# Optimization experiments

Measured on AMD Instinct MI355X. Metric: run time of the kernel, lower is better.

The kernel has to match this reference:

```python
import jax, jax.numpy as jnp
import numpy as np

LEVEL_SHAPES = ((128, 128), (64, 64), (32, 32), (16, 16))  # (H_l, W_l) per level
B, LQ, C, H, L, P, DFF = 4, 1024, 256, 8, 4, 4, 1024
DH = C // H
LSRC = sum(h * w for h, w in LEVEL_SHAPES)
NORMALIZER = np.array([[w, h] for h, w in LEVEL_SHAPES], dtype=np.float32)  # (L,2) as (W,H)


def layer_norm(x, g, b, eps=1e-5):
    m = jnp.mean(x, -1, keepdims=True)
    v = jnp.var(x, -1, keepdims=True)
    return (x - m) * jax.lax.rsqrt(v + eps) * g + b


def mha(tgt, query_pos, w_in, b_in, w_out, b_out):
    # nn.MultiheadAttention with q=k=tgt+pos, v=tgt (eval mode, no dropout)
    qk = tgt + query_pos
    q = (qk @ w_in[:C].T + b_in[:C]).reshape(B, LQ, H, DH)
    k = (qk @ w_in[C:2 * C].T + b_in[C:2 * C]).reshape(B, LQ, H, DH)
    v = (tgt @ w_in[2 * C:].T + b_in[2 * C:]).reshape(B, LQ, H, DH)
    att = jax.nn.softmax(jnp.einsum('bqhd,bkhd->bhqk', q, k) / np.float32(np.sqrt(DH)), axis=-1)
    o = jnp.einsum('bhqk,bkhd->bqhd', att, v).reshape(B, LQ, C)
    return o @ w_out.T + b_out


def ms_deform_attn(query, ref, src, off_w, off_b, aw_w, aw_b, val_w, val_b, out_w, out_b):
    value = (src @ val_w.T + val_b).reshape(B, LSRC, H, DH)
    offsets = (query @ off_w.T + off_b).reshape(B, LQ, H, L, P, 2)
    aw = jax.nn.softmax((query @ aw_w.T + aw_b).reshape(B, LQ, H, L * P), axis=-1)
    aw = aw.reshape(B, LQ, H, L, P)
    # sampling locations in [0,1], offsets normalized per level by (W_l, H_l)
    loc = ref[:, :, None, :, None, :] + offsets / NORMALIZER[None, None, None, :, None, :]
    out = jnp.zeros((B, LQ, H, DH), query.dtype)
    start = 0
    for l, (h, w) in enumerate(LEVEL_SHAPES):
        v = value[:, start:start + h * w].reshape(B, h, w, H, DH)
        v = v.transpose(0, 3, 1, 2, 4).reshape(B, H, h * w, DH)  # [B,H,hw,DH]
        start += h * w
        # grid_sample semantics: align_corners=False, zero padding
        x = loc[:, :, :, l, :, 0] * w - 0.5  # [B,LQ,H,P]
        y = loc[:, :, :, l, :, 1] * h - 0.5
        x0 = jnp.floor(x); y0 = jnp.floor(y)
        x0i = x0.astype(jnp.int32); y0i = y0.astype(jnp.int32)
        wx1 = x - x0; wx0 = 1.0 - wx1
        wy1 = y - y0; wy0 = 1.0 - wy1

        def gather(ix, iy):
            valid = ((ix >= 0) & (ix < w) & (iy >= 0) & (iy < h)).astype(v.dtype)
            idx = jnp.clip(iy, 0, h - 1) * w + jnp.clip(ix, 0, w - 1)
            idx = idx.transpose(0, 2, 1, 3).reshape(B, H, LQ * P)
            g = jnp.take_along_axis(v, idx[..., None], axis=2).reshape(B, H, LQ, P, DH)
            return g * valid.transpose(0, 2, 1, 3)[..., None]

        def wmul(ww):
            return ww.transpose(0, 2, 1, 3)[..., None]  # [B,H,LQ,P,1]

        s = (gather(x0i, y0i) * wmul(wx0 * wy0)
             + gather(x0i + 1, y0i) * wmul(wx1 * wy0)
             + gather(x0i, y0i + 1) * wmul(wx0 * wy1)
             + gather(x0i + 1, y0i + 1) * wmul(wx1 * wy1))
        out = out + jnp.einsum('bhqpd,bqhp->bqhd', s, aw[:, :, :, l])
    return out.reshape(B, LQ, C) @ out_w.T + out_b


def setup_inputs():
    key = jax.random.key(0)
    ks = jax.random.split(key, 16)

    def n(i, shape, s=0.02):
        return jax.random.normal(ks[i], shape, jnp.float32) * s

    z = lambda *s: jnp.zeros(s, jnp.float32)
    o = lambda *s: jnp.ones(s, jnp.float32)
    return {
        'tgt': n(0, (B, LQ, C), 1.0),
        'query_pos': n(1, (B, LQ, C), 1.0),
        'reference_points': jax.random.uniform(ks[2], (B, LQ, L, 2), jnp.float32),
        'src': n(3, (B, LSRC, C), 1.0),
        'in_w': n(4, (3 * C, C)), 'in_b': z(3 * C),
        'sa_w': n(5, (C, C)), 'sa_b': z(C),
        'off_w': n(6, (H * L * P * 2, C)), 'off_b': n(7, (H * L * P * 2,), 2.0),
        'aw_w': n(8, (H * L * P, C)), 'aw_b': z(H * L * P),
        'val_w': n(9, (C, C)), 'val_b': z(C),
        'co_w': n(10, (C, C)), 'co_b': z(C),
        'ln1_g': o(C), 'ln1_b': z(C),
        'ln2_g': o(C), 'ln2_b': z(C),
        'ln3_g': o(C), 'ln3_b': z(C),
        'f1_w': n(11, (DFF, C)), 'f1_b': z(DFF),
        'f2_w': n(12, (C, DFF)), 'f2_b': z(C),
    }


def reference(tgt, query_pos, reference_points, src, in_w, in_b, sa_w, sa_b,
              off_w, off_b, aw_w, aw_b, val_w, val_b, co_w, co_b,
              ln1_g, ln1_b, ln2_g, ln2_b, ln3_g, ln3_b,
              f1_w, f1_b, f2_w, f2_b):
    # self-attention + residual + norm2
    tgt2 = mha(tgt, query_pos, in_w, in_b, sa_w, sa_b)
    tgt = layer_norm(tgt + tgt2, ln2_g, ln2_b)
    # multi-scale deformable cross-attention + residual + norm1 (DETR path)
    tgt2 = ms_deform_attn(tgt + query_pos, reference_points, src,
                          off_w, off_b, aw_w, aw_b, val_w, val_b, co_w, co_b)
    tgt = layer_norm(tgt + tgt2, ln1_g, ln1_b)
    # FFN + residual + norm3
    tgt2 = jax.nn.relu(tgt @ f1_w.T + f1_b) @ f2_w.T + f2_b
    tgt = layer_norm(tgt + tgt2, ln3_g, ln3_b)
    return tgt
```

## Files before the change

kernel.cpp:

```cpp
#include <hip/hip_runtime.h>
#include <hip/hip_bf16.h>
#include <math.h>

#define Bv   4
#define LQv  1024
#define Cv   256
#define Hv   8
#define Lv   4
#define Pv   4
#define DFFv 1024
#define DHv  32
#define LSRCv 21760

typedef __attribute__((ext_vector_type(8))) short bhalf8;
typedef __attribute__((ext_vector_type(4))) float floatx4;

__device__ inline unsigned pk_bf16x2(float x, float y) {
    unsigned xb = __float_as_uint(x), yb = __float_as_uint(y);
    unsigned xr = (xb + 0x7FFFu + ((xb >> 16) & 1u)) >> 16;
    unsigned yr = (yb + 0x7FFFu + ((yb >> 16) & 1u)) >> 16;
    return xr | (yr << 16);
}
__device__ inline unsigned short bf16_1(float x) {
    unsigned xb = __float_as_uint(x);
    return (unsigned short)((xb + 0x7FFFu + ((xb >> 16) & 1u)) >> 16);
}
__device__ inline float ubf2f(unsigned short u) {
    return __uint_as_float(((unsigned)u) << 16);
}

__global__ __launch_bounds__(256) void cvt_weights(const float* __restrict__ in_w,
                                                   const float* __restrict__ sa_w,
                                                   const float* __restrict__ val_w,
                                                   const float* __restrict__ off_w,
                                                   const float* __restrict__ aw_w,
                                                   const float* __restrict__ co_w,
                                                   const float* __restrict__ f1_w,
                                                   const float* __restrict__ f2_w,
                                                   const float* __restrict__ off_b,
                                                   const float* __restrict__ aw_b,
                                                   unsigned short* __restrict__ wp,
                                                   float* __restrict__ cbias) {
    const size_t idx4 = (size_t)blockIdx.x * 256 + threadIdx.x;
    if (idx4 >= 253952) {
        const int t = (int)(idx4 - 253952);
        if (t < 256) cbias[t] = off_b[t];
        else if (t < 384) cbias[t] = aw_b[t - 256];
        return;
    }
    const size_t f = idx4 * 4;
    const float* src; size_t off; int K; size_t obase; int nadd = 0;
    if (f < 196608)      { src = in_w;  off = f;          K = 256;  obase = 0; }
    else if (f < 262144) { src = sa_w;  off = f - 196608; K = 256;  obase = 196608; }
    else if (f < 327680) { src = val_w; off = f - 262144; K = 256;  obase = 262144; }
    else if (f < 393216) { src = off_w; off = f - 327680; K = 256;  obase = 327680; }
    else if (f < 425984) { src = aw_w;  off = f - 393216; K = 256;  obase = 327680; nadd = 256; }
    else if (f < 491520) { src = co_w;  off = f - 425984; K = 256;  obase = 425984; }
    else if (f < 753664) { src = f1_w;  off = f - 491520; K = 256;  obase = 491520; }
    else                 { src = f2_w;  off = f - 753664; K = 1024; obase = 753664; }
    float4 v = *(const float4*)(src + off);
    const int n = (int)(off / (size_t)K) + nadd, k = (int)(off % (size_t)K);
    const size_t di = obase + ((size_t)((n >> 4) * (K >> 5) + (k >> 5))) * 512
                    + (size_t)(((k >> 3) & 3) * 128 + (n & 15) * 8 + (k & 7));
    *(uint2*)(wp + di) = (uint2){pk_bf16x2(v.x, v.y), pk_bf16x2(v.z, v.w)};
}

struct GJob {
    const float* A; const float* A2;
    const unsigned short* Wp; const float* bias;
    float* Cf; unsigned short* Ch;
    int M, N, K, relu;
};

__device__ __forceinline__ void gemm_body(unsigned short* AsBase,
                                          const float* __restrict__ A,
                                          const float* __restrict__ A2,
                                          const unsigned short* __restrict__ Wp,
                                          const float* __restrict__ bias,
                                          float* __restrict__ Cf,
                                          unsigned short* __restrict__ Ch,
                                          int N, int K, int relu, unsigned bid) {
    const unsigned nc = (unsigned)N >> 6;
    const unsigned xcd = bid & 7, j = bid >> 3;
    const unsigned cpan = j % nc, r8 = j / nc;
    const int bm = (int)((xcd + (r8 << 3)) << 6);
    const int bn = (int)(cpan << 6);
    const int tid = threadIdx.x;
    const int wid = tid >> 6, lane = tid & 63;
    const int wr = wid >> 1, wc = wid & 1;
    const int col16 = lane & 15;
    const int quad = lane >> 4;

    const int srow0 = tid >> 4;
    const int scol = (tid & 15) * 4;
    const float* asrc = A + (size_t)(bm + srow0) * K + scol;
    const float* a2src = A2 ? A2 + (size_t)(bm + srow0) * K + scol : nullptr;

    const int K32 = K >> 5;
    const unsigned short* wbase = Wp + ((size_t)((bn >> 4) + wc * 2) * K32) * 512
                                + (size_t)lane * 8;

    floatx4 acc[2][2] = {};
    float4 rv[4][2];

    auto loadA = [&](int c) {
#pragma unroll
        for (int j2 = 0; j2 < 4; ++j2)
#pragma unroll
            for (int i = 0; i < 2; ++i)
                rv[j2][i] = *(const float4*)(asrc + (size_t)(16 * j2) * K + c * 128 + 64 * i);
        if (a2src) {
#pragma unroll
            for (int j2 = 0; j2 < 4; ++j2)
#pragma unroll
                for (int i = 0; i < 2; ++i) {
                    float4 t = *(const float4*)(a2src + (size_t)(16 * j2) * K + c * 128 + 64 * i);
                    rv[j2][i].x += t.x; rv[j2][i].y += t.y;
                    rv[j2][i].z += t.z; rv[j2][i].w += t.w;
                }
        }
    };
    auto writeA = [&](int buf) {
        unsigned short* dst = AsBase + buf * (64 * 136);
#pragma unroll
        for (int j2 = 0; j2 < 4; ++j2)
#pragma unroll
            for (int i = 0; i < 2; ++i) {
                uint2 p = {pk_bf16x2(rv[j2][i].x, rv[j2][i].y),
                           pk_bf16x2(rv[j2][i].z, rv[j2][i].w)};
                *(uint2*)&dst[(srow0 + 16 * j2) * 136 + scol + 64 * i] = p;
            }
    };

    const int NC = K >> 7;
    loadA(0);
    writeA(0);

    for (int c = 0; c < NC; ++c) {
        __syncthreads();
        if (c + 1 < NC) loadA(c + 1);

        const unsigned short* ab = AsBase + (c & 1) * (64 * 136);
#pragma unroll
        for (int s = 0; s < 4; ++s) {
            bhalf8 bfr[2];
#pragma unroll
            for (int nt = 0; nt < 2; ++nt)
                bfr[nt] = *(const bhalf8*)(wbase + ((size_t)(nt * K32 + c * 4 + s)) * 512);
            bhalf8 af[2];
#pragma unroll
            for (int mt = 0; mt < 2; ++mt)
                af[mt] = *(const bhalf8*)&ab[(wr * 32 + mt * 16 + col16) * 136 + s * 32 + quad * 8];
#pragma unroll
            for (int mt = 0; mt < 2; ++mt)
#pragma unroll
                for (int nt = 0; nt < 2; ++nt)
                    acc[mt][nt] = __builtin_amdgcn_mfma_f32_16x16x32_bf16(
                        af[mt], bfr[nt], acc[mt][nt], 0, 0, 0);
        }

        if (c + 1 < NC) writeA((c + 1) & 1);
    }

#pragma unroll
    for (int mt = 0; mt < 2; ++mt) {
#pragma unroll
        for (int nt = 0; nt < 2; ++nt) {
            const int col = bn + wc * 32 + nt * 16 + col16;
            const float bv = bias[col];
#pragma unroll
            for (int i = 0; i < 4; ++i) {
                const int row = bm + wr * 32 + mt * 16 + quad * 4 + i;
                float v = acc[mt][nt][i] + bv;
                if (relu) v = fmaxf(v, 0.f);
                if (Ch) Ch[(size_t)row * N + col] = bf16_1(v);
                else    Cf[(size_t)row * N + col] = v;
            }
        }
    }
}

__global__ __launch_bounds__(256, 4) void gemm_single(const float* __restrict__ A,
                                                      const float* __restrict__ A2,
                                                      const unsigned short* __restrict__ Wp,
                                                      const float* __restrict__ bias,
                                                      float* __restrict__ Cf,
                                                      unsigned short* __restrict__ Ch,
                                                      int N, int K, int relu) {
    __shared__ __attribute__((aligned(16))) unsigned short As[2 * 64 * 136];
    gemm_body(As, A, A2, Wp, bias, Cf, Ch, N, K, relu, blockIdx.x);
}

__global__ __launch_bounds__(256, 4) void gemm_triple(GJob j0, GJob j1, GJob j2,
                                                      unsigned c0, unsigned c01) {
    __shared__ __attribute__((aligned(16))) unsigned short As[2 * 64 * 136];
    const unsigned b = blockIdx.x;
    if (b < c0) {
        gemm_body(As, j0.A, j0.A2, j0.Wp, j0.bias, j0.Cf, j0.Ch, j0.N, j0.K, j0.relu, b);
    } else if (b < c01) {
        gemm_body(As, j1.A, j1.A2, j1.Wp, j1.bias, j1.Cf, j1.Ch, j1.N, j1.K, j1.relu, b - c0);
    } else {
        gemm_body(As, j2.A, j2.A2, j2.Wp, j2.bias, j2.Cf, j2.Ch, j2.N, j2.K, j2.relu, b - c01);
    }
}

#define ATT_SCALE 0.17677669529663687f
__global__ __launch_bounds__(256, 2) void attn_mfma(const float* __restrict__ Q,
                                                    const float* __restrict__ Kb,
                                                    const float* __restrict__ Vb,
                                                    float* __restrict__ O,
                                                    int qk_stride) {
    const int b = blockIdx.z, h = blockIdx.y, qt = blockIdx.x;
    const int tid = threadIdx.x;
    const int wid = tid >> 6, lane = tid & 63;
    const int col16 = lane & 15, quad = lane >> 4;

    __shared__ unsigned short smem_us[40960];
    unsigned short* Ks = smem_us + wid * 9600;
    unsigned short* Vt = Ks + 2560;
    unsigned short* Ps = Ks + 4864;
    float* corr_s = (float*)(Ks + 9472);
    unsigned short* Qs = smem_us + 38400;

    {
        const int row = tid >> 2, part = tid & 3;
        const float* qsrc = Q + ((size_t)(b * LQv + qt * 64 + row)) * qk_stride + h * DHv + part * 8;
        float4 qa = *(const float4*)qsrc;
        float4 qb2 = *(const float4*)(qsrc + 4);
        uint4 qp = {pk_bf16x2(qa.x * ATT_SCALE, qa.y * ATT_SCALE),
                    pk_bf16x2(qa.z * ATT_SCALE, qa.w * ATT_SCALE),
                    pk_bf16x2(qb2.x * ATT_SCALE, qb2.y * ATT_SCALE),
                    pk_bf16x2(qb2.z * ATT_SCALE, qb2.w * ATT_SCALE)};
        *(uint4*)&Qs[row * 40 + part * 8] = qp;
    }
    __syncthreads();
    bhalf8 qfr[4];
#pragma unroll
    for (int j = 0; j < 4; ++j)
        qfr[j] = *(const bhalf8*)&Qs[(j * 16 + col16) * 40 + quad * 8];

    float m_state[4] = {-1e30f, -1e30f, -1e30f, -1e30f};
    float l_state[4] = {0.f, 0.f, 0.f, 0.f};
    floatx4 acc_o[4][2] = {};
    const int dd = lane & 31, half = lane >> 5;

    const float* kbase = Kb + ((size_t)(b * LQv + wid * 256)) * qk_stride + h * DHv;
    const float* vbase = Vb + ((size_t)(b * LQv + wid * 256)) * Cv + h * DHv;

#pragma unroll 1
    for (int t = 0; t < 4; ++t) {
        {
            const float* ks = kbase + (size_t)(t * 64 + lane) * qk_stride;
            float4 f0 = *(const float4*)(ks + 0),  f1 = *(const float4*)(ks + 4);
            float4 f2 = *(const float4*)(ks + 8),  f3 = *(const float4*)(ks + 12);
            float4 f4 = *(const float4*)(ks + 16), f5 = *(const float4*)(ks + 20);
            float4 f6 = *(const float4*)(ks + 24), f7 = *(const float4*)(ks + 28);
            uint4 p0 = {pk_bf16x2(f0.x, f0.y), pk_bf16x2(f0.z, f0.w),
                        pk_bf16x2(f1.x, f1.y), pk_bf16x2(f1.z, f1.w)};
            uint4 p1 = {pk_bf16x2(f2.x, f2.y), pk_bf16x2(f2.z, f2.w),
                        pk_bf16x2(f3.x, f3.y), pk_bf16x2(f3.z, f3.w)};
            uint4 p2 = {pk_bf16x2(f4.x, f4.y), pk_bf16x2(f4.z, f4.w),
                        pk_bf16x2(f5.x, f5.y), pk_bf16x2(f5.z, f5.w)};
            uint4 p3 = {pk_bf16x2(f6.x, f6.y), pk_bf16x2(f6.z, f6.w),
                        pk_bf16x2(f7.x, f7.y), pk_bf16x2(f7.z, f7.w)};
            *(uint4*)&Ks[lane * 40 + 0]  = p0;
            *(uint4*)&Ks[lane * 40 + 8]  = p1;
            *(uint4*)&Ks[lane * 40 + 16] = p2;
            *(uint4*)&Ks[lane * 40 + 24] = p3;
        }
        {
            const float* vs = vbase + (size_t)(t * 64 + half * 32) * Cv + dd;
#pragma unroll
            for (int j4 = 0; j4 < 8; ++j4) {
                float g0 = vs[(j4 * 4 + 0) * Cv], g1 = vs[(j4 * 4 + 1) * Cv];
                float g2 = vs[(j4 * 4 + 2) * Cv], g3 = vs[(j4 * 4 + 3) * Cv];
                uint2 vp = {pk_bf16x2(g0, g1), pk_bf16x2(g2, g3)};
                *(uint2*)&Vt[dd * 72 + half * 32 + j4 * 4] = vp;
            }
        }

        floatx4 accs[4][4] = {};
        bhalf8 af[4];
#pragma unroll
        for (int kf = 0; kf < 4; ++kf)
            af[kf] = *(const bhalf8*)&Ks[(kf * 16 + col16) * 40 + quad * 8];
#pragma unroll
        for (int kf = 0; kf < 4; ++kf)
#pragma unroll
            for (int qf = 0; qf < 4; ++qf)
                accs[kf][qf] = __builtin_amdgcn_mfma_f32_16x16x32_bf16(
                    af[kf], qfr[qf], accs[kf][qf], 0, 0, 0);

#pragma unroll
        for (int qf = 0; qf < 4; ++qf) {
            float tmax = -1e30f;
#pragma unroll
            for (int kf = 0; kf < 4; ++kf) {
                tmax = fmaxf(tmax, fmaxf(fmaxf(accs[kf][qf][0], accs[kf][qf][1]),
                                         fmaxf(accs[kf][qf][2], accs[kf][qf][3])));
            }
            tmax = fmaxf(tmax, __shfl_xor(tmax, 16));
            tmax = fmaxf(tmax, __shfl_xor(tmax, 32));
            float mnew = fmaxf(m_state[qf], tmax);
            float cr = __expf(m_state[qf] - mnew);
            m_state[qf] = mnew;
            float psum = 0.f;
#pragma unroll
            for (int kf = 0; kf < 4; ++kf) {
                float p0 = __expf(accs[kf][qf][0] - mnew);
                float p1 = __expf(accs[kf][qf][1] - mnew);
                float p2 = __expf(accs[kf][qf][2] - mnew);
                float p3 = __expf(accs[kf][qf][3] - mnew);
                psum += (p0 + p1) + (p2 + p3);
                uint2 pp = {pk_bf16x2(p0, p1), pk_bf16x2(p2, p3)};
                *(uint2*)&Ps[(qf * 16 + col16) * 72 + kf * 16 + quad * 4] = pp;
            }
            psum += __shfl_xor(psum, 16);
            psum += __shfl_xor(psum, 32);
            l_state[qf] = l_state[qf] * cr + psum;
            if (quad == 0) corr_s[qf * 16 + col16] = cr;
        }

#pragma unroll
        for (int mf = 0; mf < 4; ++mf) {
            float4 cv = *(const float4*)&corr_s[mf * 16 + quad * 4];
#pragma unroll
            for (int nf = 0; nf < 2; ++nf) {
                acc_o[mf][nf][0] *= cv.x;
                acc_o[mf][nf][1] *= cv.y;
                acc_o[mf][nf][2] *= cv.z;
                acc_o[mf][nf][3] *= cv.w;
            }
        }
#pragma unroll
        for (int ks2 = 0; ks2 < 2; ++ks2) {
            bhalf8 pf[4], vf[2];
#pragma unroll
            for (int mf = 0; mf < 4; ++mf)
                pf[mf] = *(const bhalf8*)&Ps[(mf * 16 + col16) * 72 + ks2 * 32 + quad * 8];
#pragma unroll
            for (int nf = 0; nf < 2; ++nf)
                vf[nf] = *(const bhalf8*)&Vt[(nf * 16 + col16) * 72 + ks2 * 32 + quad * 8];
#pragma unroll
            for (int mf = 0; mf < 4; ++mf)
#pragma unroll
                for (int nf = 0; nf < 2; ++nf)
                    acc_o[mf][nf] = __builtin_amdgcn_mfma_f32_16x16x32_bf16(
                        pf[mf], vf[nf], acc_o[mf][nf], 0, 0, 0);
        }
    }

    __syncthreads();
    float* mbuf = (float*)smem_us;
    float* lbuf = mbuf + 256;
    float* obuf = lbuf + 256;
    if (quad == 0) {
#pragma unroll
        for (int qf = 0; qf < 4; ++qf) {
            mbuf[wid * 64 + qf * 16 + col16] = m_state[qf];
            lbuf[wid * 64 + qf * 16 + col16] = l_state[qf];
        }
    }
#pragma unroll
    for (int mf = 0; mf < 4; ++mf)
#pragma unroll
        for (int nf = 0; nf < 2; ++nf)
#pragma unroll
            for (int i = 0; i < 4; ++i)
                obuf[wid * 2048 + (mf * 16 + quad * 4 + i) * 32 + nf * 16 + col16] =
                    acc_o[mf][nf][i];
    __syncthreads();
    {
        const int q = tid >> 2, dg = (tid & 3) * 8;
        float m0 = mbuf[q], m1 = mbuf[64 + q], m2 = mbuf[128 + q], m3 = mbuf[192 + q];
        float gm = fmaxf(fmaxf(m0, m1), fmaxf(m2, m3));
        float e0 = __expf(m0 - gm), e1 = __expf(m1 - gm);
        float e2 = __expf(m2 - gm), e3 = __expf(m3 - gm);
        float lt = lbuf[q] * e0 + lbuf[64 + q] * e1 + lbuf[128 + q] * e2 + lbuf[192 + q] * e3;
        float inv = 1.f / lt;
        const float* o0 = obuf + q * 32 + dg;
        float* orow = O + ((size_t)(b * LQv + qt * 64 + q)) * Cv + h * DHv + dg;
        float ov[8];
#pragma unroll
        for (int d = 0; d < 8; ++d)
            ov[d] = (o0[d] * e0 + o0[2048 + d] * e1 + o0[4096 + d] * e2 + o0[6144 + d] * e3) * inv;
        *(float4*)(orow) = make_float4(ov[0], ov[1], ov[2], ov[3]);
        *(float4*)(orow + 4) = make_float4(ov[4], ov[5], ov[6], ov[7]);
    }
}

__global__ __launch_bounds__(256) void deform_sample(const unsigned short* __restrict__ value,
                                                     const float* __restrict__ oab,
                                                     const float* __restrict__ ref,
                                                     float* __restrict__ out) {
    const int bq = blockIdx.x;
    const int b = bq >> 10;
    const int tid = threadIdx.x;
    const int h = tid >> 5, d = tid & 31;

    const float* aw = oab + (size_t)bq * 384 + 256 + h * 16;
    float w[16];
    float mx = -1e30f;
#pragma unroll
    for (int j = 0; j < 16; ++j) { w[j] = aw[j]; mx = fmaxf(mx, w[j]); }
    float ssum = 0.f;
#pragma unroll
    for (int j = 0; j < 16; ++j) { w[j] = __expf(w[j] - mx); ssum += w[j]; }
    float invs = 1.f / ssum;

    const float* op = oab + (size_t)bq * 384 + h * 32;
    const float* rp = ref + (size_t)bq * (Lv * 2);

    const int starts[4] = {0, 16384, 20480, 21504};
    const int WHl[4] = {128, 64, 32, 16};

    float acc = 0.f;
#pragma unroll 1
    for (int l = 0; l < 4; ++l) {
        const int wl = WHl[l];
        const float rx = rp[l * 2 + 0], ry = rp[l * 2 + 1];
        const unsigned short* vb0 = value + ((size_t)b * LSRCv + starts[l]) * Cv + h * DHv + d;
#pragma unroll 1
        for (int p = 0; p < 4; ++p) {
            float ox = op[l * 8 + p * 2 + 0], oy = op[l * 8 + p * 2 + 1];
            float x = rx * (float)wl + ox - 0.5f;
            float y = ry * (float)wl + oy - 0.5f;
            float fx0 = floorf(x), fy0 = floorf(y);
            int x0 = (int)fx0, y0 = (int)fy0;
            float tx = x - fx0, ty = y - fy0;
            float w00 = (1.f - tx) * (1.f - ty);
            float w10 = tx * (1.f - ty);
            float w01 = (1.f - tx) * ty;
            float w11 = tx * ty;
            float s = 0.f;
            bool xin0 = (x0 >= 0) & (x0 < wl);
            bool xin1 = (x0 + 1 >= 0) & (x0 + 1 < wl);
            bool yin0 = (y0 >= 0) & (y0 < wl);
            bool yin1 = (y0 + 1 >= 0) & (y0 + 1 < wl);
            if (yin0) {
                if (xin0) s = fmaf(w00, ubf2f(vb0[(size_t)(y0 * wl + x0) * Cv]), s);
                if (xin1) s = fmaf(w10, ubf2f(vb0[(size_t)(y0 * wl + x0 + 1) * Cv]), s);
            }
            if (yin1) {
                if (xin0) s = fmaf(w01, ubf2f(vb0[(size_t)((y0 + 1) * wl + x0) * Cv]), s);
                if (xin1) s = fmaf(w11, ubf2f(vb0[(size_t)((y0 + 1) * wl + x0 + 1) * Cv]), s);
            }
            acc = fmaf(w[l * 4 + p] * invs, s, acc);
        }
    }
    out[(size_t)bq * Cv + h * DHv + d] = acc;
}

__global__ __launch_bounds__(256) void ln_residual(const float* __restrict__ x,
                                                   const float* __restrict__ r,
                                                   const float* __restrict__ g,
                                                   const float* __restrict__ bta,
                                                   float* __restrict__ out) {
    const int row = blockIdx.x;
    const int tid = threadIdx.x;
    float v = x[(size_t)row * Cv + tid] + r[(size_t)row * Cv + tid];
    float s = v, sq = v * v;
#pragma unroll
    for (int off = 32; off > 0; off >>= 1) {
        s  += __shfl_down(s, off, 64);
        sq += __shfl_down(sq, off, 64);
    }
    __shared__ float ss[4], sqq[4];
    int wid = tid >> 6;
    if ((tid & 63) == 0) { ss[wid] = s; sqq[wid] = sq; }
    __syncthreads();
    __shared__ float meansh, rstdsh;
    if (tid == 0) {
        float S = ss[0] + ss[1] + ss[2] + ss[3];
        float Q = sqq[0] + sqq[1] + sqq[2] + sqq[3];
        float mean = S * (1.f / Cv);
        float var = Q * (1.f / Cv) - mean * mean;
        meansh = mean;
        rstdsh = rsqrtf(var + 1e-5f);
    }
    __syncthreads();
    out[(size_t)row * Cv + tid] = (v - meansh) * rstdsh * g[tid] + bta[tid];
}

extern "C" void kernel_launch(void* const* d_in, const int* in_sizes, int n_in,
                              void* d_out, int out_size, void* d_ws, size_t ws_size,
                              hipStream_t stream) {
    const float* tgt       = (const float*)d_in[0];
    const float* query_pos = (const float*)d_in[1];
    const float* ref_pts   = (const float*)d_in[2];
    const float* src       = (const float*)d_in[3];
    const float* in_w      = (const float*)d_in[4];
    const float* in_b      = (const float*)d_in[5];
    const float* sa_w      = (const float*)d_in[6];
    const float* sa_b      = (const float*)d_in[7];
    const float* off_w     = (const float*)d_in[8];
    const float* off_b     = (const float*)d_in[9];
    const float* aw_w      = (const float*)d_in[10];
    const float* aw_b      = (const float*)d_in[11];
    const float* val_w     = (const float*)d_in[12];
    const float* val_b     = (const float*)d_in[13];
    const float* co_w      = (const float*)d_in[14];
    const float* co_b      = (const float*)d_in[15];
    const float* ln1_g     = (const float*)d_in[16];
    const float* ln1_b     = (const float*)d_in[17];
    const float* ln2_g     = (const float*)d_in[18];
    const float* ln2_b     = (const float*)d_in[19];
    const float* ln3_g     = (const float*)d_in[20];
    const float* ln3_b     = (const float*)d_in[21];
    const float* f1_w      = (const float*)d_in[22];
    const float* f1_b      = (const float*)d_in[23];
    const float* f2_w      = (const float*)d_in[24];
    const float* f2_b      = (const float*)d_in[25];

    const int M0  = Bv * LQv * Cv;
    const int VSZ = Bv * LSRCv * Cv;
    float* ws = (float*)d_ws;

    float* big    = ws;
    float* qkbuf  = big;
    float* vb     = big + (size_t)2 * M0;
    float* ob     = big + (size_t)3 * M0;
    unsigned short* value16 = (unsigned short*)(big + (size_t)4 * M0);
    unsigned short* wb = (unsigned short*)(big + (size_t)20000000);
    float* cbias  = big + (size_t)20510000;
    float* tgt_a  = ws + (size_t)VSZ;
    float* oabuf  = tgt_a + M0;
    float* sampled= oabuf + (size_t)Bv * LQv * 384;
    float* tgt_b  = sampled + M0;
    float* hidden = tgt_b + M0;
    float* tmp    = hidden + (size_t)Bv * LQv * DFFv;

    const size_t WB_IN = 0, WB_SA = 196608, WB_VAL = 262144, WB_OA = 327680,
                 WB_CO = 425984, WB_F1 = 491520, WB_F2 = 753664;

    const int Mq = Bv * LQv;
    dim3 blk256(256);

    cvt_weights<<<dim3(993), blk256, 0, stream>>>(
        in_w, sa_w, val_w, off_w, aw_w, co_w, f1_w, f2_w, off_b, aw_b, wb, cbias);

    {
        GJob jqk = {tgt, query_pos, wb + WB_IN, in_b, qkbuf, nullptr,
                    Mq, 512, Cv, 0};
        GJob jv  = {tgt, nullptr, wb + WB_IN + 131072, in_b + 2 * Cv, vb, nullptr,
                    Mq, Cv, Cv, 0};
        GJob jval= {src, nullptr, wb + WB_VAL, val_b, nullptr, value16,
                    Bv * LSRCv, Cv, Cv, 0};
        const unsigned c0 = (Mq / 64) * (512 / 64);
        const unsigned c1 = (Mq / 64) * (Cv / 64);
        const unsigned c2 = ((Bv * LSRCv) / 64) * (Cv / 64);
        gemm_triple<<<dim3(c0 + c1 + c2), blk256, 0, stream>>>(
            jqk, jv, jval, c0, c0 + c1);
    }

    attn_mfma<<<dim3(LQv / 64, Hv, Bv), blk256, 0, stream>>>(qkbuf, qkbuf + 256, vb, ob, 512);

    gemm_single<<<dim3((Mq / 64) * (Cv / 64)), blk256, 0, stream>>>(
        ob, nullptr, wb + WB_SA, sa_b, tmp, nullptr, Cv, Cv, 0);
    ln_residual<<<dim3(Mq), blk256, 0, stream>>>(tgt, tmp, ln2_g, ln2_b, tgt_a);

    gemm_single<<<dim3((Mq / 64) * (384 / 64)), blk256, 0, stream>>>(
        tgt_a, query_pos, wb + WB_OA, cbias, oabuf, nullptr, 384, Cv, 0);

    deform_sample<<<dim3(Bv * LQv), blk256, 0, stream>>>(value16, oabuf, ref_pts, sampled);

    gemm_single<<<dim3((Mq / 64) * (Cv / 64)), blk256, 0, stream>>>(
        sampled, nullptr, wb + WB_CO, co_b, tmp, nullptr, Cv, Cv, 0);
    ln_residual<<<dim3(Mq), blk256, 0, stream>>>(tgt_a, tmp, ln1_g, ln1_b, tgt_b);

    gemm_single<<<dim3((Mq / 64) * (DFFv / 64)), blk256, 0, stream>>>(
        tgt_b, nullptr, wb + WB_F1, f1_b, hidden, nullptr, DFFv, Cv, 1);
    gemm_single<<<dim3((Mq / 64) * (Cv / 64)), blk256, 0, stream>>>(
        hidden, nullptr, wb + WB_F2, f2_b, tmp, nullptr, Cv, DFFv, 0);
    ln_residual<<<dim3(Mq), blk256, 0, stream>>>(tgt_b, tmp, ln3_g, ln3_b, (float*)d_out);
}
```

Measured before the change: 362.6 us.

## Fuse output-projection GEMMs with residual add and LayerNorm epilogue

Adds a gemm_ln kernel where each block computes a full 32x256 row tile, then adds bias and residual and does the LayerNorm reduction in-block through shuffles and shared memory. It replaces the three gemm_single + ln_residual pairs, which removes three launches and the round trip of the fp32 tmp buffer. In exchange the grid drops to 128 blocks of 32 rows, which may underfill the GPU's compute units, and the K=1024 FFN GEMM is now split across fewer blocks.

```diff
diff --git a/kernel.cpp b/kernel.cpp
--- a/kernel.cpp
+++ b/kernel.cpp
@@ -202,6 +202,153 @@
     } else {
         gemm_body(As, j2.A, j2.A2, j2.Wp, j2.bias, j2.Cf, j2.Ch, j2.N, j2.K, j2.relu, b - c01);
     }
+}
+
+__global__ __launch_bounds__(256, 2) void gemm_ln(const float* __restrict__ A,
+                                                  const unsigned short* __restrict__ Wp,
+                                                  const float* __restrict__ bias,
+                                                  const float* __restrict__ res,
+                                                  const float* __restrict__ g,
+                                                  const float* __restrict__ beta,
+                                                  float* __restrict__ out,
+                                                  int K) {
+    __shared__ __attribute__((aligned(16))) unsigned short As[2][32 * 136];
+    const int bm = blockIdx.x * 32;
+    const int tid = threadIdx.x;
+    const int wid = tid >> 6, lane = tid & 63;
+    const int col16 = lane & 15, quad = lane >> 4;
+    const int wc = wid;
+
+    const int srow = tid >> 3;
+    const int sc16 = (tid & 7) * 16;
+    const float* asrc = A + (size_t)(bm + srow) * K + sc16;
+
+    const int K32 = K >> 5;
+    const unsigned short* wbase = Wp + (size_t)(wc * 4) * K32 * 512 + (size_t)lane * 8;
+
+    floatx4 acc[2][4] = {};
+    float4 rv[4];
+
+    auto loadA = [&](int c) {
+#pragma unroll
+        for (int j = 0; j < 4; ++j)
+            rv[j] = *(const float4*)(asrc + c * 128 + j * 4);
+    };
+    auto writeA = [&](int buf) {
+#pragma unroll
+        for (int j = 0; j < 4; ++j) {
+            uint2 p = {pk_bf16x2(rv[j].x, rv[j].y), pk_bf16x2(rv[j].z, rv[j].w)};
+            *(uint2*)&As[buf][srow * 136 + sc16 + j * 4] = p;
+        }
+    };
+
+    const int NC = K >> 7;
+    loadA(0);
+    writeA(0);
+
+    for (int c = 0; c < NC; ++c) {
+        __syncthreads();
+        if (c + 1 < NC) loadA(c + 1);
+
+        const unsigned short* ab = As[c & 1];
+#pragma unroll
+        for (int s = 0; s < 4; ++s) {
+            bhalf8 bfr[4];
+#pragma unroll
+            for (int nt = 0; nt < 4; ++nt)
+                bfr[nt] = *(const bhalf8*)(wbase + ((size_t)(nt * K32 + c * 4 + s)) * 512);
+            bhalf8 af[2];
+#pragma unroll
+            for (int mt = 0; mt < 2; ++mt)
+                af[mt] = *(const bhalf8*)&ab[(mt * 16 + col16) * 136 + s * 32 + quad * 8];
+#pragma unroll
+            for (int mt = 0; mt < 2; ++mt)
+#pragma unroll
+                for (int nt = 0; nt < 4; ++nt)
+                    acc[mt][nt] = __builtin_amdgcn_mfma_f32_16x16x32_bf16(
+                        af[mt], bfr[nt], acc[mt][nt], 0, 0, 0);
+        }
+
+        if (c + 1 < NC) writeA((c + 1) & 1);
+    }
+
+    float bias_r[4];
+#pragma unroll
+    for (int nt = 0; nt < 4; ++nt) bias_r[nt] = bias[wc * 64 + nt * 16 + col16];
+
+    float s_[2][4], q_[2][4];
+#pragma unroll
+    for (int mt = 0; mt < 2; ++mt)
+#pragma unroll
+        for (int i = 0; i < 4; ++i) { s_[mt][i] = 0.f; q_[mt][i] = 0.f; }
+
+#pragma unroll
+    for (int mt = 0; mt < 2; ++mt)
+#pragma unroll
+        for (int i = 0; i < 4; ++i) {
+            const int row = bm + mt * 16 + quad * 4 + i;
+#pragma unroll
+            for (int nt = 0; nt < 4; ++nt) {
+                float r = res[(size_t)row * 256 + wc * 64 + nt * 16 + col16];
+                float v = acc[mt][nt][i] + bias_r[nt] + r;
+                acc[mt][nt][i] = v;
+                s_[mt][i] += v;
+                q_[mt][i] = fmaf(v, v, q_[mt][i]);
+            }
+        }
+
+#pragma unroll
+    for (int mt = 0; mt < 2; ++mt)
+#pragma unroll
+        for (int i = 0; i < 4; ++i) {
+#pragma unroll
+            for (int off = 1; off < 16; off <<= 1) {
+                s_[mt][i] += __shfl_xor(s_[mt][i], off, 64);
+                q_[mt][i] += __shfl_xor(q_[mt][i], off, 64);
+            }
+        }
+
+    __syncthreads();
+    float* red = (float*)As;
+    if (col16 == 0) {
+#pragma unroll
+        for (int mt = 0; mt < 2; ++mt)
+#pragma unroll
+            for (int i = 0; i < 4; ++i) {
+                red[wid * 32 + mt * 16 + quad * 4 + i] = s_[mt][i];
+                red[128 + wid * 32 + mt * 16 + quad * 4 + i] = q_[mt][i];
+            }
+    }
+    __syncthreads();
+    float* mean_s = red + 256;
+    float* rstd_s = red + 288;
+    if (tid < 32) {
+        float S = red[tid] + red[32 + tid] + red[64 + tid] + red[96 + tid];
+        float Q = red[128 + tid] + red[160 + tid] + red[192 + tid] + red[224 + tid];
+        float mean = S * (1.f / 256.f);
+        float var = Q * (1.f / 256.f) - mean * mean;
+        mean_s[tid] = mean;
+        rstd_s[tid] = rsqrtf(var + 1e-5f);
+    }
+    __syncthreads();
+
+    float g_r[4], b_r[4];
+#pragma unroll
+    for (int nt = 0; nt < 4; ++nt) {
+        g_r[nt] = g[wc * 64 + nt * 16 + col16];
+        b_r[nt] = beta[wc * 64 + nt * 16 + col16];
+    }
+#pragma unroll
+    for (int mt = 0; mt < 2; ++mt)
+#pragma unroll
+        for (int i = 0; i < 4; ++i) {
+            const int rl = mt * 16 + quad * 4 + i;
+            const float mn = mean_s[rl], rs = rstd_s[rl];
+#pragma unroll
+            for (int nt = 0; nt < 4; ++nt)
+                out[(size_t)(bm + rl) * 256 + wc * 64 + nt * 16 + col16] =
+                    (acc[mt][nt][i] - mn) * rs * g_r[nt] + b_r[nt];
+        }
 }
 
 #define ATT_SCALE 0.17677669529663687f
@@ -449,37 +596,6 @@
         }
     }
     out[(size_t)bq * Cv + h * DHv + d] = acc;
-}
-
-__global__ __launch_bounds__(256) void ln_residual(const float* __restrict__ x,
-                                                   const float* __restrict__ r,
-                                                   const float* __restrict__ g,
-                                                   const float* __restrict__ bta,
-                                                   float* __restrict__ out) {
-    const int row = blockIdx.x;
-    const int tid = threadIdx.x;
-    float v = x[(size_t)row * Cv + tid] + r[(size_t)row * Cv + tid];
-    float s = v, sq = v * v;
-#pragma unroll
-    for (int off = 32; off > 0; off >>= 1) {
-        s  += __shfl_down(s, off, 64);
-        sq += __shfl_down(sq, off, 64);
-    }
-    __shared__ float ss[4], sqq[4];
-    int wid = tid >> 6;
-    if ((tid & 63) == 0) { ss[wid] = s; sqq[wid] = sq; }
-    __syncthreads();
-    __shared__ float meansh, rstdsh;
-    if (tid == 0) {
-        float S = ss[0] + ss[1] + ss[2] + ss[3];
-        float Q = sqq[0] + sqq[1] + sqq[2] + sqq[3];
-        float mean = S * (1.f / Cv);
-        float var = Q * (1.f / Cv) - mean * mean;
-        meansh = mean;
-        rstdsh = rsqrtf(var + 1e-5f);
-    }
-    __syncthreads();
-    out[(size_t)row * Cv + tid] = (v - meansh) * rstdsh * g[tid] + bta[tid];
 }
 
 extern "C" void kernel_launch(void* const* d_in, const int* in_sizes, int n_in,
@@ -528,7 +644,6 @@
     float* sampled= oabuf + (size_t)Bv * LQv * 384;
     float* tgt_b  = sampled + M0;
     float* hidden = tgt_b + M0;
-    float* tmp    = hidden + (size_t)Bv * LQv * DFFv;
 
     const size_t WB_IN = 0, WB_SA = 196608, WB_VAL = 262144, WB_OA = 327680,
                  WB_CO = 425984, WB_F1 = 491520, WB_F2 = 753664;
@@ -555,22 +670,20 @@
 
     attn_mfma<<<dim3(LQv / 64, Hv, Bv), blk256, 0, stream>>>(qkbuf, qkbuf + 256, vb, ob, 512);
 
-    gemm_single<<<dim3((Mq / 64) * (Cv / 64)), blk256, 0, stream>>>(
-        ob, nullptr, wb + WB_SA, sa_b, tmp, nullptr, Cv, Cv, 0);
-    ln_residual<<<dim3(Mq), blk256, 0, stream>>>(tgt, tmp, ln2_g, ln2_b, tgt_a);
+    gemm_ln<<<dim3(Mq / 32), blk256, 0, stream>>>(
+        ob, wb + WB_SA, sa_b, tgt, ln2_g, ln2_b, tgt_a, Cv);
 
     gemm_single<<<dim3((Mq / 64) * (384 / 64)), blk256, 0, stream>>>(
         tgt_a, query_pos, wb + WB_OA, cbias, oabuf, nullptr, 384, Cv, 0);
 
     deform_sample<<<dim3(Bv * LQv), blk256, 0, stream>>>(value16, oabuf, ref_pts, sampled);
 
-    gemm_single<<<dim3((Mq / 64) * (Cv / 64)), blk256, 0, stream>>>(
-        sampled, nullptr, wb + WB_CO, co_b, tmp, nullptr, Cv, Cv, 0);
-    ln_residual<<<dim3(Mq), blk256, 0, stream>>>(tgt_a, tmp, ln1_g, ln1_b, tgt_b);
+    gemm_ln<<<dim3(Mq / 32), blk256, 0, stream>>>(
+        sampled, wb + WB_CO, co_b, tgt_a, ln1_g, ln1_b, tgt_b, Cv);
 
     gemm_single<<<dim3((Mq / 64) * (DFFv / 64)), blk256, 0, stream>>>(
         tgt_b, nullptr, wb + WB_F1, f1_b, hidden, nullptr, DFFv, Cv, 1);
-    gemm_single<<<dim3((Mq / 64) * (Cv / 64)), blk256, 0, stream>>>(
-        hidden, nullptr, wb + WB_F2, f2_b, tmp, nullptr, Cv, DFFv, 0);
-    ln_residual<<<dim3(Mq), blk256, 0, stream>>>(tgt_b, tmp, ln3_g, ln3_b, (float*)d_out);
-}
+
+    gemm_ln<<<dim3(Mq / 32), blk256, 0, stream>>>(
+        hidden, wb + WB_F2, f2_b, tgt_b, ln3_g, ln3_b, (float*)d_out, DFFv);
+}
```

Measured after the change: 349.4 us. 1.04x faster.
